# Kernel tuning notes

Measured on AMD Instinct MI355X. Metric: run time of the kernel, lower is better.

The kernel has to match this reference:

```python
import jax, jax.numpy as jnp
import numpy as np

NUM_EXPERTS = 8
HIDDEN = 1024
INTER = 1024
BATCH = 2
SEQ = 1024
TOP_K = 2
SWIGLU_ALPHA = 1.702
LIMIT = 7.0


def setup_inputs() -> dict:
    key = jax.random.key(0)
    ks = jax.random.split(key, 7)
    hidden_states = jax.random.normal(ks[0], (BATCH, SEQ, HIDDEN), jnp.float32)
    router_indices = jax.random.randint(ks[1], (BATCH * SEQ, TOP_K), 0, NUM_EXPERTS)
    routing_weights = jax.nn.softmax(
        jax.random.normal(ks[2], (BATCH * SEQ, NUM_EXPERTS), jnp.float32), axis=-1)
    scale = 0.02
    gate_up_proj = jax.random.normal(ks[3], (NUM_EXPERTS, HIDDEN, 2 * INTER), jnp.float32) * scale
    gate_up_proj_bias = jax.random.normal(ks[4], (NUM_EXPERTS, 2 * INTER), jnp.float32) * scale
    down_proj = jax.random.normal(ks[5], (NUM_EXPERTS, INTER, HIDDEN), jnp.float32) * scale
    down_proj_bias = jax.random.normal(ks[6], (NUM_EXPERTS, HIDDEN), jnp.float32) * scale
    return {
        "hidden_states": hidden_states,
        "router_indices": router_indices,
        "routing_weights": routing_weights,
        "gate_up_proj": gate_up_proj,
        "gate_up_proj_bias": gate_up_proj_bias,
        "down_proj": down_proj,
        "down_proj_bias": down_proj_bias,
    }


def _grouped_mm(x, w, expert_ids):
    """Grouped GEMM: y[t] = x[t] @ w[expert_ids[t]].

    x: [T, K], w: [E, K, N], expert_ids: [T] int.
    Reference form via one-hot masking (exact equivalent of torch._grouped_mm
    on expert-sorted tokens); guaranteed jit- and grad-safe.
    """
    onehot = jax.nn.one_hot(expert_ids, w.shape[0], dtype=x.dtype)  # [T, E]
    y_all = jnp.einsum('tk,ekn->etn', x, w)                         # [E, T, N]
    return jnp.einsum('te,etn->tn', onehot, y_all)                  # [T, N]


def _gpt_oss_swiglu(x):
    gate = jnp.minimum(x[..., ::2], LIMIT)
    up = jnp.clip(x[..., 1::2], -LIMIT, LIMIT)
    glu = gate * jax.nn.sigmoid(gate * SWIGLU_ALPHA)
    return (up + 1.0) * glu


def reference(hidden_states, router_indices, routing_weights,
              gate_up_proj, gate_up_proj_bias, down_proj, down_proj_bias):
    B = hidden_states.shape[0]
    H = hidden_states.shape[-1]
    x = hidden_states.reshape(-1, H)                       # [M, H]
    M = x.shape[0]
    top_k = router_indices.shape[1]
    num_experts = gate_up_proj.shape[0]

    # routing_weights is [M, num_experts] -> gather the top-k weights
    topk_weights = jnp.take_along_axis(routing_weights, router_indices, axis=1)  # [M, K]

    flat_experts = router_indices.reshape(-1)              # [T = M*K]
    sort_idx = jnp.argsort(flat_experts)                   # expert-sorted order
    sorted_pos = sort_idx // top_k                         # token id per slot
    expert_sorted = flat_experts[sort_idx]                 # [T]
    grouped = x[sorted_pos]                                # [T, H]

    gate_up = _grouped_mm(grouped, gate_up_proj, expert_sorted)
    gate_up = gate_up + gate_up_proj_bias[expert_sorted]   # per-expert bias
    inter = _gpt_oss_swiglu(gate_up)                       # [T, I]

    down = _grouped_mm(inter, down_proj, expert_sorted)
    down = down + down_proj_bias[expert_sorted]            # [T, H]
    down = down * topk_weights.reshape(-1)[sort_idx][:, None]

    out = jnp.zeros((M, H), x.dtype).at[sorted_pos].add(down)  # scatter-add combine
    return out.reshape(B, -1, H)
```

## Files before the change

kernel.cpp:

```cpp
#include <hip/hip_runtime.h>

#define NE 8
#define NH 1024
#define NI 1024
#define NGU 2048
#define MTOK 2048
#define TSLOT 4096

#define MAXT64 80
#define MAXT128 40

typedef short s16x8 __attribute__((ext_vector_type(8)));
typedef float f32x4 __attribute__((ext_vector_type(4)));
typedef unsigned short u16;

#define WS_SEG      0
#define WS_DESC64   64
#define WS_DESC128  384
#define WS_SLOT     1024
#define WS_POS      17408
#define WS_INTER    33792
#define WS_AREG     8422400UL
#define WS_WREG     25199616UL
#define WS_DB_OFF   16777216UL
#define WS_NEED_FAST 58754048UL

__device__ inline u16 f2bf(float f) {
    unsigned u = __builtin_bit_cast(unsigned, f);
    u += 0x7fffu + ((u >> 16) & 1u);
    return (u16)(u >> 16);
}

__device__ inline void lds_dma16(const u16* g, u16* l) {
    __builtin_amdgcn_global_load_lds(
        (const __attribute__((address_space(1))) unsigned int*)g,
        (__attribute__((address_space(3))) unsigned int*)l, 16, 0, 0);
}

__device__ inline int lds_off(int row, int blk) {
    return (row << 7) | (((blk ^ (row & 7)) & 7) << 4);
}

__global__ void k_build(const int* __restrict__ ridx, int* __restrict__ seg,
                        int* __restrict__ d64, int* __restrict__ d128,
                        int* __restrict__ slot_of, int* __restrict__ pos_of) {
    __shared__ int cnt[NE];
    __shared__ int cur[NE];
    int tid = threadIdx.x;
    if (tid < NE) cnt[tid] = 0;
    __syncthreads();
    for (int s = tid; s < TSLOT; s += blockDim.x) atomicAdd(&cnt[ridx[s] & 7], 1);
    __syncthreads();
    if (tid == 0) {
        int a = 0;
        for (int e = 0; e < NE; ++e) { seg[e] = a; cur[e] = a; a += cnt[e]; }
        seg[NE] = a;
        int nt = 0;
        for (int e = 0; e < NE; ++e)
            for (int m0 = 0; m0 < cnt[e]; m0 += 64) d64[nt++] = (e << 16) | (m0 / 64);
        for (; nt < MAXT64; ++nt) d64[nt] = -1;
        nt = 0;
        for (int e = 0; e < NE; ++e)
            for (int m0 = 0; m0 < cnt[e]; m0 += 128) d128[nt++] = (e << 16) | (m0 / 128);
        for (; nt < MAXT128; ++nt) d128[nt] = -1;
    }
    __syncthreads();
    for (int s = tid; s < TSLOT; s += blockDim.x) {
        int e = ridx[s] & 7;
        int p = atomicAdd(&cur[e], 1);
        slot_of[p] = s;
        pos_of[s] = p;
    }
}

__global__ __launch_bounds__(256) void k_gather(const float* __restrict__ x,
                                                const int* __restrict__ slot_of,
                                                u16* __restrict__ A) {
    int r = blockIdx.x;
    int token = slot_of[r] >> 1;
    float4 v = ((const float4*)(x + (size_t)token * NH))[threadIdx.x];
    ushort4 o;
    o.x = f2bf(v.x); o.y = f2bf(v.y); o.z = f2bf(v.z); o.w = f2bf(v.w);
    ((ushort4*)(A + (size_t)r * NH))[threadIdx.x] = o;
}

__global__ __launch_bounds__(256) void k_tr(const float* __restrict__ W,
                                            u16* __restrict__ WT, int K, int N) {
    __shared__ u16 T[64][66];
    int tid = threadIdx.x;
    const float* in = W + (size_t)blockIdx.z * K * N;
    u16* out = WT + (size_t)blockIdx.z * N * K;
    int n0 = blockIdx.x * 64, k0 = blockIdx.y * 64;
#pragma unroll
    for (int p = 0; p < 2; ++p) {
        int kr = p * 32 + (tid >> 4) * 2;
        int nc = (tid & 15) * 4;
        const float* r0 = in + (size_t)(k0 + kr) * N + n0 + nc;
        float4 v0 = *(const float4*)r0;
        float4 v1 = *(const float4*)(r0 + N);
#pragma unroll
        for (int i = 0; i < 4; ++i) {
            unsigned lo = f2bf(((const float*)&v0)[i]);
            unsigned hi = f2bf(((const float*)&v1)[i]);
            *(unsigned*)&T[nc + i][kr] = lo | (hi << 16);
        }
    }
    __syncthreads();
#pragma unroll
    for (int p = 0; p < 2; ++p) {
        int idx = p * 256 + tid;
        int nr = idx >> 3, kc = (idx & 7) * 8;
        unsigned q0 = *(const unsigned*)&T[nr][kc + 0];
        unsigned q1 = *(const unsigned*)&T[nr][kc + 2];
        unsigned q2 = *(const unsigned*)&T[nr][kc + 4];
        unsigned q3 = *(const unsigned*)&T[nr][kc + 6];
        uint4 vv = {q0, q1, q2, q3};
        *(uint4*)(out + (size_t)(n0 + nr) * K + k0 + kc) = vv;
    }
}

__global__ __launch_bounds__(256) void k_gateup_f(
        const u16* __restrict__ A,
        const u16* __restrict__ wt,
        const float* __restrict__ bias,
        const int* __restrict__ seg, const int* __restrict__ desc,
        u16* __restrict__ inter) {
    int d = desc[blockIdx.x];
    if (d < 0) return;
    int e = d >> 16, mt = d & 0xffff;
    int seg0 = seg[e], Te = seg[e + 1] - seg0, m0 = mt * 128;

    __shared__ __align__(16) u16 As[128 * 64];
    __shared__ __align__(16) u16 Bs[64 * 64];

    int tid = threadIdx.x;
    int lane = tid & 63, w = tid >> 6;
    int ml = lane & 15, kq = lane >> 4;
    int wm = w >> 1, wn = w & 1;
    int n0 = blockIdx.y * 64;
    const u16* wte = wt + (size_t)e * NGU * NH;
    int dr = lane >> 3, db = (lane & 7) ^ dr;

    f32x4 zero = {0.f, 0.f, 0.f, 0.f};
    f32x4 acc[4][2];
#pragma unroll
    for (int i = 0; i < 4; ++i) { acc[i][0] = zero; acc[i][1] = zero; }

    for (int kb = 0; kb < NH; kb += 64) {
        __syncthreads();
#pragma unroll
        for (int c = 0; c < 4; ++c) {
            int gr = seg0 + m0 + c * 32 + w * 8 + dr;
            if (gr > TSLOT - 1) gr = TSLOT - 1;
            lds_dma16(A + (size_t)gr * NH + kb + db * 8, As + c * 2048 + w * 512);
        }
#pragma unroll
        for (int c = 0; c < 2; ++c) {
            int row = c * 32 + w * 8 + dr;
            lds_dma16(wte + (size_t)(n0 + row) * NH + kb + db * 8, Bs + c * 2048 + w * 512);
        }
        __syncthreads();

#pragma unroll
        for (int kk = 0; kk < 64; kk += 32) {
            s16x8 af[4], bf[2];
#pragma unroll
            for (int i = 0; i < 4; ++i)
                af[i] = *(const s16x8*)((char*)As + lds_off(wm * 64 + i * 16 + ml, (kk >> 3) + kq));
#pragma unroll
            for (int i = 0; i < 2; ++i)
                bf[i] = *(const s16x8*)((char*)Bs + lds_off(wn * 32 + i * 16 + ml, (kk >> 3) + kq));
#pragma unroll
            for (int mi = 0; mi < 4; ++mi)
#pragma unroll
                for (int ni = 0; ni < 2; ++ni)
                    acc[mi][ni] = __builtin_amdgcn_mfma_f32_16x16x32_bf16(
                        af[mi], bf[ni], acc[mi][ni], 0, 0, 0);
        }
    }

#pragma unroll
    for (int ni = 0; ni < 2; ++ni) {
        int n = n0 + wn * 32 + ni * 16 + ml;
        float bv = bias[e * NGU + n];
#pragma unroll
        for (int mi = 0; mi < 4; ++mi) {
#pragma unroll
            for (int r = 0; r < 4; ++r) {
                float v = acc[mi][ni][r] + bv;
                float pr = __shfl_xor(v, 1, 64);
                float g = (lane & 1) ? pr : v;
                float u = (lane & 1) ? v : pr;
                g = fminf(g, 7.0f);
                u = fminf(fmaxf(u, -7.0f), 7.0f);
                float glu = g / (1.0f + __expf(-1.702f * g));
                float y = (u + 1.0f) * glu;
                int mloc = wm * 64 + mi * 16 + kq * 4 + r;
                if (!(lane & 1) && (m0 + mloc) < Te)
                    inter[(size_t)(seg0 + m0 + mloc) * NI + (n >> 1)] = f2bf(y);
            }
        }
    }
}

__global__ __launch_bounds__(256) void k_down_f(
        const u16* __restrict__ inter,
        const u16* __restrict__ wt,
        const float* __restrict__ bias,
        const int* __restrict__ seg, const int* __restrict__ desc,
        float* __restrict__ dA,
        float* __restrict__ dB) {
    int d = desc[blockIdx.x];
    if (d < 0) return;
    int e = d >> 16, mt = d & 0xffff;
    int seg0 = seg[e], Te = seg[e + 1] - seg0, m0 = mt * 128;
    int kz = blockIdx.z;

    __shared__ __align__(16) u16 As[128 * 64];
    __shared__ __align__(16) u16 Bs[64 * 64];

    int tid = threadIdx.x;
    int lane = tid & 63, w = tid >> 6;
    int ml = lane & 15, kq = lane >> 4;
    int wm = w >> 1, wn = w & 1;
    int n0 = blockIdx.y * 64;
    const u16* wte = wt + (size_t)e * NH * NI;
    int dr = lane >> 3, db = (lane & 7) ^ dr;

    f32x4 zero = {0.f, 0.f, 0.f, 0.f};
    f32x4 acc[4][2];
#pragma unroll
    for (int i = 0; i < 4; ++i) { acc[i][0] = zero; acc[i][1] = zero; }

    int kbeg = kz * (NI / 2);
    for (int kb = kbeg; kb < kbeg + NI / 2; kb += 64) {
        __syncthreads();
#pragma unroll
        for (int c = 0; c < 4; ++c) {
            int gr = seg0 + m0 + c * 32 + w * 8 + dr;
            if (gr > TSLOT - 1) gr = TSLOT - 1;
            lds_dma16(inter + (size_t)gr * NI + kb + db * 8, As + c * 2048 + w * 512);
        }
#pragma unroll
        for (int c = 0; c < 2; ++c) {
            int row = c * 32 + w * 8 + dr;
            lds_dma16(wte + (size_t)(n0 + row) * NI + kb + db * 8, Bs + c * 2048 + w * 512);
        }
        __syncthreads();

#pragma unroll
        for (int kk = 0; kk < 64; kk += 32) {
            s16x8 af[4], bf[2];
#pragma unroll
            for (int i = 0; i < 4; ++i)
                af[i] = *(const s16x8*)((char*)As + lds_off(wm * 64 + i * 16 + ml, (kk >> 3) + kq));
#pragma unroll
            for (int i = 0; i < 2; ++i)
                bf[i] = *(const s16x8*)((char*)Bs + lds_off(wn * 32 + i * 16 + ml, (kk >> 3) + kq));
#pragma unroll
            for (int mi = 0; mi < 4; ++mi)
#pragma unroll
                for (int ni = 0; ni < 2; ++ni)
                    acc[mi][ni] = __builtin_amdgcn_mfma_f32_16x16x32_bf16(
                        af[mi], bf[ni], acc[mi][ni], 0, 0, 0);
        }
    }

    float* dst = kz ? dB : dA;
    float bv[2];
#pragma unroll
    for (int ni = 0; ni < 2; ++ni)
        bv[ni] = (kz == 0) ? bias[e * NH + n0 + wn * 32 + ni * 16 + ml] : 0.0f;

#pragma unroll
    for (int mi = 0; mi < 4; ++mi) {
#pragma unroll
        for (int r = 0; r < 4; ++r) {
            int mloc = wm * 64 + mi * 16 + kq * 4 + r;
            if ((m0 + mloc) < Te) {
                size_t row = (size_t)(seg0 + m0 + mloc);
#pragma unroll
                for (int ni = 0; ni < 2; ++ni) {
                    int n = n0 + wn * 32 + ni * 16 + ml;
                    dst[row * NH + n] = acc[mi][ni][r] + bv[ni];
                }
            }
        }
    }
}

__global__ __launch_bounds__(256) void k_comb(
        const float* __restrict__ dA, const float* __restrict__ dB,
        const float* __restrict__ rw, const int* __restrict__ ridx,
        const int* __restrict__ pos_of, float* __restrict__ out) {
    int t = blockIdx.x;
    int h = threadIdx.x * 4;
    float4 s = {0.f, 0.f, 0.f, 0.f};
#pragma unroll
    for (int k = 0; k < 2; ++k) {
        int slot = t * 2 + k;
        int e = ridx[slot] & 7;
        float wgt = rw[t * NE + e];
        size_t r = (size_t)pos_of[slot];
        float4 a = *(const float4*)(dA + r * NH + h);
        float4 b = *(const float4*)(dB + r * NH + h);
        s.x += wgt * (a.x + b.x);
        s.y += wgt * (a.y + b.y);
        s.z += wgt * (a.z + b.z);
        s.w += wgt * (a.w + b.w);
    }
    *(float4*)(out + (size_t)t * NH + h) = s;
}

__global__ __launch_bounds__(256) void k_gateup_s(
        const float* __restrict__ x, const float* __restrict__ w,
        const float* __restrict__ bias,
        const int* __restrict__ seg, const int* __restrict__ desc,
        const int* __restrict__ slot_of, u16* __restrict__ inter) {
    int d = desc[blockIdx.x];
    if (d < 0) return;
    int e = d >> 16, mt = d & 0xffff;
    int seg0 = seg[e], Te = seg[e + 1] - seg0, m0 = mt * 64;
    __shared__ u16 As[64 * 40];
    __shared__ int tok[64];
    int tid = threadIdx.x;
    if (tid < 64) {
        int m = m0 + tid;
        tok[tid] = (m < Te) ? (slot_of[seg0 + m] >> 1) : -1;
    }
    __syncthreads();
    int lane = tid & 63, wave = tid >> 6;
    int arow = tid >> 2, acol = (tid & 3) * 8;
    int ta = tok[arow];
    int kq = lane >> 4, ml = lane & 15;
    int nb = blockIdx.y * 128 + wave * 32;
    const float* wp = w + (size_t)e * NH * NGU;
    f32x4 zero = {0.f, 0.f, 0.f, 0.f};
    f32x4 acc[4][2];
#pragma unroll
    for (int i = 0; i < 4; ++i) { acc[i][0] = zero; acc[i][1] = zero; }
    for (int kb = 0; kb < NH; kb += 32) {
        float4 a0 = {0, 0, 0, 0}, a1 = {0, 0, 0, 0};
        if (ta >= 0) {
            const float* xp = x + (size_t)ta * NH + kb + acol;
            a0 = *(const float4*)xp; a1 = *(const float4*)(xp + 4);
        }
        s16x8 av;
        av[0] = (short)f2bf(a0.x); av[1] = (short)f2bf(a0.y);
        av[2] = (short)f2bf(a0.z); av[3] = (short)f2bf(a0.w);
        av[4] = (short)f2bf(a1.x); av[5] = (short)f2bf(a1.y);
        av[6] = (short)f2bf(a1.z); av[7] = (short)f2bf(a1.w);
        __syncthreads();
        *(s16x8*)&As[arow * 40 + acol] = av;
        __syncthreads();
        s16x8 afr[4];
#pragma unroll
        for (int msi = 0; msi < 4; ++msi)
            afr[msi] = *(const s16x8*)&As[(msi * 16 + ml) * 40 + kq * 8];
        s16x8 bfr[2];
#pragma unroll
        for (int s = 0; s < 2; ++s) {
            const float* bp = wp + (size_t)(kb + kq * 8) * NGU + nb + s * 16 + ml;
#pragma unroll
            for (int j = 0; j < 8; ++j) bfr[s][j] = (short)f2bf(bp[(size_t)j * NGU]);
        }
#pragma unroll
        for (int msi = 0; msi < 4; ++msi)
#pragma unroll
            for (int s = 0; s < 2; ++s)
                acc[msi][s] = __builtin_amdgcn_mfma_f32_16x16x32_bf16(
                    afr[msi], bfr[s], acc[msi][s], 0, 0, 0);
    }
#pragma unroll
    for (int s = 0; s < 2; ++s) {
        int n = nb + s * 16 + ml;
        float bv = bias[e * NGU + n];
#pragma unroll
        for (int msi = 0; msi < 4; ++msi) {
#pragma unroll
            for (int r = 0; r < 4; ++r) {
                float v = acc[msi][s][r] + bv;
                float pr = __shfl_xor(v, 1, 64);
                float g = (lane & 1) ? pr : v;
                float u = (lane & 1) ? v : pr;
                g = fminf(g, 7.0f);
                u = fminf(fmaxf(u, -7.0f), 7.0f);
                float glu = g / (1.0f + __expf(-1.702f * g));
                float y = (u + 1.0f) * glu;
                int mrow = m0 + msi * 16 + kq * 4 + r;
                if (!(lane & 1) && mrow < Te)
                    inter[(size_t)(seg0 + mrow) * NI + (n >> 1)] = f2bf(y);
            }
        }
    }
}

__global__ __launch_bounds__(256) void k_down_s(
        const u16* __restrict__ inter, const float* __restrict__ w,
        const float* __restrict__ bias, const float* __restrict__ rw,
        const int* __restrict__ seg, const int* __restrict__ desc,
        const int* __restrict__ slot_of, float* __restrict__ out) {
    int d = desc[blockIdx.x];
    if (d < 0) return;
    int e = d >> 16, mt = d & 0xffff;
    int seg0 = seg[e], Te = seg[e + 1] - seg0, m0 = mt * 64;
    __shared__ u16 As[64 * 40];
    int tid = threadIdx.x;
    int lane = tid & 63, wave = tid >> 6;
    int arow = tid >> 2, acol = (tid & 3) * 8;
    bool avalid = (m0 + arow) < Te;
    int kq = lane >> 4, ml = lane & 15;
    int nb = blockIdx.y * 128 + wave * 32;
    const float* wp = w + (size_t)e * NI * NH;
    f32x4 zero = {0.f, 0.f, 0.f, 0.f};
    f32x4 acc[4][2];
#pragma unroll
    for (int i = 0; i < 4; ++i) { acc[i][0] = zero; acc[i][1] = zero; }
    for (int kb = 0; kb < NI; kb += 32) {
        s16x8 av = {0, 0, 0, 0, 0, 0, 0, 0};
        if (avalid) av = *(const s16x8*)(inter + (size_t)(seg0 + m0 + arow) * NI + kb + acol);
        __syncthreads();
        *(s16x8*)&As[arow * 40 + acol] = av;
        __syncthreads();
        s16x8 afr[4];
#pragma unroll
        for (int msi = 0; msi < 4; ++msi)
            afr[msi] = *(const s16x8*)&As[(msi * 16 + ml) * 40 + kq * 8];
        s16x8 bfr[2];
#pragma unroll
        for (int s = 0; s < 2; ++s) {
            const float* bp = wp + (size_t)(kb + kq * 8) * NH + nb + s * 16 + ml;
#pragma unroll
            for (int j = 0; j < 8; ++j) bfr[s][j] = (short)f2bf(bp[(size_t)j * NH]);
        }
#pragma unroll
        for (int msi = 0; msi < 4; ++msi)
#pragma unroll
            for (int s = 0; s < 2; ++s)
                acc[msi][s] = __builtin_amdgcn_mfma_f32_16x16x32_bf16(
                    afr[msi], bfr[s], acc[msi][s], 0, 0, 0);
    }
    float bv[2];
    bv[0] = bias[e * NH + nb + ml];
    bv[1] = bias[e * NH + nb + 16 + ml];
#pragma unroll
    for (int msi = 0; msi < 4; ++msi) {
#pragma unroll
        for (int r = 0; r < 4; ++r) {
            int mrow = m0 + msi * 16 + kq * 4 + r;
            if (mrow < Te) {
                int slot = slot_of[seg0 + mrow];
                int token = slot >> 1;
                float wgt = rw[token * NE + e];
#pragma unroll
                for (int s = 0; s < 2; ++s) {
                    int n = nb + s * 16 + ml;
                    atomicAdd(&out[(size_t)token * NH + n], (acc[msi][s][r] + bv[s]) * wgt);
                }
            }
        }
    }
}

extern "C" void kernel_launch(void* const* d_in, const int* in_sizes, int n_in,
                              void* d_out, int out_size, void* d_ws, size_t ws_size,
                              hipStream_t stream) {
    const float* x   = (const float*)d_in[0];
    const int*   ri  = (const int*)d_in[1];
    const float* rw  = (const float*)d_in[2];
    const float* wgu = (const float*)d_in[3];
    const float* bgu = (const float*)d_in[4];
    const float* wd  = (const float*)d_in[5];
    const float* bd  = (const float*)d_in[6];
    float* out = (float*)d_out;

    char* ws = (char*)d_ws;
    int* seg     = (int*)(ws + WS_SEG);
    int* d64     = (int*)(ws + WS_DESC64);
    int* d128    = (int*)(ws + WS_DESC128);
    int* slot_of = (int*)(ws + WS_SLOT);
    int* pos_of  = (int*)(ws + WS_POS);
    u16* inter   = (u16*)(ws + WS_INTER);

    hipLaunchKernelGGL(k_build, dim3(1), dim3(256), 0, stream, ri, seg, d64, d128,
                       slot_of, pos_of);

    if (ws_size >= WS_NEED_FAST) {
        u16*   aReg = (u16*)(ws + WS_AREG);
        float* dA   = (float*)(ws + WS_AREG);
        u16*   wReg = (u16*)(ws + WS_WREG);
        float* dB   = (float*)(ws + WS_WREG + WS_DB_OFF);

        hipLaunchKernelGGL(k_tr, dim3(NGU / 64, NH / 64, NE), dim3(256), 0, stream,
                           wgu, wReg, NH, NGU);
        hipLaunchKernelGGL(k_gather, dim3(TSLOT), dim3(256), 0, stream, x, slot_of, aReg);
        hipLaunchKernelGGL(k_gateup_f, dim3(MAXT128, NGU / 64), dim3(256), 0, stream,
                           aReg, wReg, bgu, seg, d128, inter);
        hipLaunchKernelGGL(k_tr, dim3(NH / 64, NI / 64, NE), dim3(256), 0, stream,
                           wd, wReg, NI, NH);
        hipLaunchKernelGGL(k_down_f, dim3(MAXT128, NH / 64, 2), dim3(256), 0, stream,
                           inter, wReg, bd, seg, d128, dA, dB);
        hipLaunchKernelGGL(k_comb, dim3(MTOK), dim3(256), 0, stream,
                           dA, dB, rw, ri, pos_of, out);
    } else {
        hipMemsetAsync(out, 0, (size_t)MTOK * NH * sizeof(float), stream);
        hipLaunchKernelGGL(k_gateup_s, dim3(MAXT64, NGU / 128), dim3(256), 0, stream,
                           x, wgu, bgu, seg, d64, slot_of, inter);
        hipLaunchKernelGGL(k_down_s, dim3(MAXT64, NH / 128), dim3(256), 0, stream,
                           inter, wd, bd, rw, seg, d64, slot_of, out);
    }
}
```

Measured before the change: 229.4 us.

## Fuse weight bf16 conversion into GEMM staging and combine via atomic scatter

Removes the separate weight transpose/convert kernels; each GEMM block now loads fp32 weights directly and packs them to bf16 into swizzled shared memory. The down projection drops its K-split and the separate combine kernel, instead applying routing weights and atomically adding into a zeroed output. This eliminates a large intermediate write/read of converted weights and two launches, at the cost of reading fp32 weights (twice the bytes) repeatedly per M-tile, less down-GEMM parallelism, and atomic contention.

```diff
diff --git a/kernel.cpp b/kernel.cpp
--- a/kernel.cpp
+++ b/kernel.cpp
@@ -21,9 +21,7 @@
 #define WS_POS      17408
 #define WS_INTER    33792
 #define WS_AREG     8422400UL
-#define WS_WREG     25199616UL
-#define WS_DB_OFF   16777216UL
-#define WS_NEED_FAST 58754048UL
+#define WS_NEED_FAST 16811008UL
 
 __device__ inline u16 f2bf(float f) {
     unsigned u = __builtin_bit_cast(unsigned, f);
@@ -31,6 +29,12 @@
     return (u16)(u >> 16);
 }
 
+__device__ inline unsigned cvt_pk_bf16(float lo, float hi) {
+    unsigned r;
+    asm("v_cvt_pk_bf16_f32 %0, %1, %2" : "=v"(r) : "v"(lo), "v"(hi));
+    return r;
+}
+
 __device__ inline void lds_dma16(const u16* g, u16* l) {
     __builtin_amdgcn_global_load_lds(
         (const __attribute__((address_space(1))) unsigned int*)g,
@@ -39,6 +43,28 @@
 
 __device__ inline int lds_off(int row, int blk) {
     return (row << 7) | (((blk ^ (row & 7)) & 7) << 4);
+}
+
+template<int N>
+__device__ inline void stageB(const float* __restrict__ wt, u16* __restrict__ Bs, int tid) {
+    int lane = tid & 63, w = tid >> 6;
+    int kr = 2 * (lane & 3) + 8 * ((lane >> 2) & 3);
+    int nc = ((lane >> 4) << 2) + (w << 4);
+    const float* r0 = wt + (size_t)kr * N + nc;
+    float4 v0 = *(const float4*)r0;
+    float4 v1 = *(const float4*)(r0 + N);
+    const float* r1 = r0 + (size_t)32 * N;
+    float4 v2 = *(const float4*)r1;
+    float4 v3 = *(const float4*)(r1 + N);
+    int c0 = kr >> 3, kb2 = (kr & 7) << 1;
+#pragma unroll
+    for (int i = 0; i < 4; ++i) {
+        int n = nc + i;
+        unsigned pk0 = cvt_pk_bf16(((const float*)&v0)[i], ((const float*)&v1)[i]);
+        *(unsigned*)((char*)Bs + (n << 7) + (((c0 ^ (n & 7)) & 7) << 4) + kb2) = pk0;
+        unsigned pk1 = cvt_pk_bf16(((const float*)&v2)[i], ((const float*)&v3)[i]);
+        *(unsigned*)((char*)Bs + (n << 7) + ((((c0 + 4) ^ (n & 7)) & 7) << 4) + kb2) = pk1;
+    }
 }
 
 __global__ void k_build(const int* __restrict__ ridx, int* __restrict__ seg,
@@ -84,44 +110,9 @@
     ((ushort4*)(A + (size_t)r * NH))[threadIdx.x] = o;
 }
 
-__global__ __launch_bounds__(256) void k_tr(const float* __restrict__ W,
-                                            u16* __restrict__ WT, int K, int N) {
-    __shared__ u16 T[64][66];
-    int tid = threadIdx.x;
-    const float* in = W + (size_t)blockIdx.z * K * N;
-    u16* out = WT + (size_t)blockIdx.z * N * K;
-    int n0 = blockIdx.x * 64, k0 = blockIdx.y * 64;
-#pragma unroll
-    for (int p = 0; p < 2; ++p) {
-        int kr = p * 32 + (tid >> 4) * 2;
-        int nc = (tid & 15) * 4;
-        const float* r0 = in + (size_t)(k0 + kr) * N + n0 + nc;
-        float4 v0 = *(const float4*)r0;
-        float4 v1 = *(const float4*)(r0 + N);
-#pragma unroll
-        for (int i = 0; i < 4; ++i) {
-            unsigned lo = f2bf(((const float*)&v0)[i]);
-            unsigned hi = f2bf(((const float*)&v1)[i]);
-            *(unsigned*)&T[nc + i][kr] = lo | (hi << 16);
-        }
-    }
-    __syncthreads();
-#pragma unroll
-    for (int p = 0; p < 2; ++p) {
-        int idx = p * 256 + tid;
-        int nr = idx >> 3, kc = (idx & 7) * 8;
-        unsigned q0 = *(const unsigned*)&T[nr][kc + 0];
-        unsigned q1 = *(const unsigned*)&T[nr][kc + 2];
-        unsigned q2 = *(const unsigned*)&T[nr][kc + 4];
-        unsigned q3 = *(const unsigned*)&T[nr][kc + 6];
-        uint4 vv = {q0, q1, q2, q3};
-        *(uint4*)(out + (size_t)(n0 + nr) * K + k0 + kc) = vv;
-    }
-}
-
 __global__ __launch_bounds__(256) void k_gateup_f(
         const u16* __restrict__ A,
-        const u16* __restrict__ wt,
+        const float* __restrict__ W,
         const float* __restrict__ bias,
         const int* __restrict__ seg, const int* __restrict__ desc,
         u16* __restrict__ inter) {
@@ -138,7 +129,7 @@
     int ml = lane & 15, kq = lane >> 4;
     int wm = w >> 1, wn = w & 1;
     int n0 = blockIdx.y * 64;
-    const u16* wte = wt + (size_t)e * NGU * NH;
+    const float* we = W + (size_t)e * NH * NGU;
     int dr = lane >> 3, db = (lane & 7) ^ dr;
 
     f32x4 zero = {0.f, 0.f, 0.f, 0.f};
@@ -154,11 +145,7 @@
             if (gr > TSLOT - 1) gr = TSLOT - 1;
             lds_dma16(A + (size_t)gr * NH + kb + db * 8, As + c * 2048 + w * 512);
         }
-#pragma unroll
-        for (int c = 0; c < 2; ++c) {
-            int row = c * 32 + w * 8 + dr;
-            lds_dma16(wte + (size_t)(n0 + row) * NH + kb + db * 8, Bs + c * 2048 + w * 512);
-        }
+        stageB<NGU>(we + (size_t)kb * NGU + n0, Bs, tid);
         __syncthreads();
 
 #pragma unroll
@@ -205,26 +192,40 @@
 
 __global__ __launch_bounds__(256) void k_down_f(
         const u16* __restrict__ inter,
-        const u16* __restrict__ wt,
+        const float* __restrict__ W,
         const float* __restrict__ bias,
+        const float* __restrict__ rw,
         const int* __restrict__ seg, const int* __restrict__ desc,
-        float* __restrict__ dA,
-        float* __restrict__ dB) {
+        const int* __restrict__ slot_of,
+        float* __restrict__ out) {
     int d = desc[blockIdx.x];
     if (d < 0) return;
     int e = d >> 16, mt = d & 0xffff;
     int seg0 = seg[e], Te = seg[e + 1] - seg0, m0 = mt * 128;
-    int kz = blockIdx.z;
 
     __shared__ __align__(16) u16 As[128 * 64];
     __shared__ __align__(16) u16 Bs[64 * 64];
+    __shared__ int tokS[128];
+    __shared__ float wgtS[128];
 
     int tid = threadIdx.x;
+    if (tid < 128) {
+        int m = m0 + tid;
+        if (m < Te) {
+            int token = slot_of[seg0 + m] >> 1;
+            tokS[tid] = token;
+            wgtS[tid] = rw[token * NE + e];
+        } else {
+            tokS[tid] = 0;
+            wgtS[tid] = 0.0f;
+        }
+    }
+
     int lane = tid & 63, w = tid >> 6;
     int ml = lane & 15, kq = lane >> 4;
     int wm = w >> 1, wn = w & 1;
     int n0 = blockIdx.y * 64;
-    const u16* wte = wt + (size_t)e * NH * NI;
+    const float* we = W + (size_t)e * NI * NH;
     int dr = lane >> 3, db = (lane & 7) ^ dr;
 
     f32x4 zero = {0.f, 0.f, 0.f, 0.f};
@@ -232,8 +233,7 @@
 #pragma unroll
     for (int i = 0; i < 4; ++i) { acc[i][0] = zero; acc[i][1] = zero; }
 
-    int kbeg = kz * (NI / 2);
-    for (int kb = kbeg; kb < kbeg + NI / 2; kb += 64) {
+    for (int kb = 0; kb < NI; kb += 64) {
         __syncthreads();
 #pragma unroll
         for (int c = 0; c < 4; ++c) {
@@ -241,11 +241,7 @@
             if (gr > TSLOT - 1) gr = TSLOT - 1;
             lds_dma16(inter + (size_t)gr * NI + kb + db * 8, As + c * 2048 + w * 512);
         }
-#pragma unroll
-        for (int c = 0; c < 2; ++c) {
-            int row = c * 32 + w * 8 + dr;
-            lds_dma16(wte + (size_t)(n0 + row) * NI + kb + db * 8, Bs + c * 2048 + w * 512);
-        }
+        stageB<NH>(we + (size_t)kb * NH + n0, Bs, tid);
         __syncthreads();
 
 #pragma unroll
@@ -266,11 +262,10 @@
         }
     }
 
-    float* dst = kz ? dB : dA;
     float bv[2];
 #pragma unroll
     for (int ni = 0; ni < 2; ++ni)
-        bv[ni] = (kz == 0) ? bias[e * NH + n0 + wn * 32 + ni * 16 + ml] : 0.0f;
+        bv[ni] = bias[e * NH + n0 + wn * 32 + ni * 16 + ml];
 
 #pragma unroll
     for (int mi = 0; mi < 4; ++mi) {
@@ -278,38 +273,16 @@
         for (int r = 0; r < 4; ++r) {
             int mloc = wm * 64 + mi * 16 + kq * 4 + r;
             if ((m0 + mloc) < Te) {
-                size_t row = (size_t)(seg0 + m0 + mloc);
+                int token = tokS[mloc];
+                float wgt = wgtS[mloc];
 #pragma unroll
                 for (int ni = 0; ni < 2; ++ni) {
                     int n = n0 + wn * 32 + ni * 16 + ml;
-                    dst[row * NH + n] = acc[mi][ni][r] + bv[ni];
+                    atomicAdd(&out[(size_t)token * NH + n], (acc[mi][ni][r] + bv[ni]) * wgt);
                 }
             }
         }
     }
-}
-
-__global__ __launch_bounds__(256) void k_comb(
-        const float* __restrict__ dA, const float* __restrict__ dB,
-        const float* __restrict__ rw, const int* __restrict__ ridx,
-        const int* __restrict__ pos_of, float* __restrict__ out) {
-    int t = blockIdx.x;
-    int h = threadIdx.x * 4;
-    float4 s = {0.f, 0.f, 0.f, 0.f};
-#pragma unroll
-    for (int k = 0; k < 2; ++k) {
-        int slot = t * 2 + k;
-        int e = ridx[slot] & 7;
-        float wgt = rw[t * NE + e];
-        size_t r = (size_t)pos_of[slot];
-        float4 a = *(const float4*)(dA + r * NH + h);
-        float4 b = *(const float4*)(dB + r * NH + h);
-        s.x += wgt * (a.x + b.x);
-        s.y += wgt * (a.y + b.y);
-        s.z += wgt * (a.z + b.z);
-        s.w += wgt * (a.w + b.w);
-    }
-    *(float4*)(out + (size_t)t * NH + h) = s;
 }
 
 __global__ __launch_bounds__(256) void k_gateup_s(
@@ -484,26 +457,16 @@
 
     hipLaunchKernelGGL(k_build, dim3(1), dim3(256), 0, stream, ri, seg, d64, d128,
                        slot_of, pos_of);
+    hipMemsetAsync(out, 0, (size_t)MTOK * NH * sizeof(float), stream);
 
     if (ws_size >= WS_NEED_FAST) {
-        u16*   aReg = (u16*)(ws + WS_AREG);
-        float* dA   = (float*)(ws + WS_AREG);
-        u16*   wReg = (u16*)(ws + WS_WREG);
-        float* dB   = (float*)(ws + WS_WREG + WS_DB_OFF);
-
-        hipLaunchKernelGGL(k_tr, dim3(NGU / 64, NH / 64, NE), dim3(256), 0, stream,
-                           wgu, wReg, NH, NGU);
+        u16* aReg = (u16*)(ws + WS_AREG);
         hipLaunchKernelGGL(k_gather, dim3(TSLOT), dim3(256), 0, stream, x, slot_of, aReg);
         hipLaunchKernelGGL(k_gateup_f, dim3(MAXT128, NGU / 64), dim3(256), 0, stream,
-                           aReg, wReg, bgu, seg, d128, inter);
-        hipLaunchKernelGGL(k_tr, dim3(NH / 64, NI / 64, NE), dim3(256), 0, stream,
-                           wd, wReg, NI, NH);
-        hipLaunchKernelGGL(k_down_f, dim3(MAXT128, NH / 64, 2), dim3(256), 0, stream,
-                           inter, wReg, bd, seg, d128, dA, dB);
-        hipLaunchKernelGGL(k_comb, dim3(MTOK), dim3(256), 0, stream,
-                           dA, dB, rw, ri, pos_of, out);
+                           aReg, wgu, bgu, seg, d128, inter);
+        hipLaunchKernelGGL(k_down_f, dim3(MAXT128, NH / 64), dim3(256), 0, stream,
+                           inter, wd, bd, rw, seg, d128, slot_of, out);
     } else {
-        hipMemsetAsync(out, 0, (size_t)MTOK * NH * sizeof(float), stream);
         hipLaunchKernelGGL(k_gateup_s, dim3(MAXT64, NGU / 128), dim3(256), 0, stream,
                            x, wgu, bgu, seg, d64, slot_of, inter);
         hipLaunchKernelGGL(k_down_s, dim3(MAXT64, NH / 128), dim3(256), 0, stream,
```

After: 269.7 us. +17.6%, slower.

## Widen GEMM N-tile to 128 and fuse weighted combine into down kernel via atomics

Applied to the files above, without the earlier changes.

Both bf16 grouped GEMMs move from 128x64 to 128x128 output tiles, so each wave now holds a 4x4 MFMA accumulator grid and each loaded A tile is reused across twice as many columns. The down projection drops its split-K over two halves and the separate fp32 partial buffers. It now applies the routing weight and scatter-adds straight into the output with atomicAdd, which removes the k_comb kernel and its round trip through global memory. In exchange the output needs a memset, there are fewer blocks for parallelism, register pressure is higher, and the fp32 atomics make the summation order nondeterministic.

```diff
diff --git a/kernel.cpp b/kernel.cpp
--- a/kernel.cpp
+++ b/kernel.cpp
@@ -22,7 +22,6 @@
 #define WS_INTER    33792
 #define WS_AREG     8422400UL
 #define WS_WREG     25199616UL
-#define WS_DB_OFF   16777216UL
 #define WS_NEED_FAST 58754048UL
 
 __device__ inline u16 f2bf(float f) {
@@ -131,20 +130,22 @@
     int seg0 = seg[e], Te = seg[e + 1] - seg0, m0 = mt * 128;
 
     __shared__ __align__(16) u16 As[128 * 64];
-    __shared__ __align__(16) u16 Bs[64 * 64];
+    __shared__ __align__(16) u16 Bs[128 * 64];
 
     int tid = threadIdx.x;
     int lane = tid & 63, w = tid >> 6;
     int ml = lane & 15, kq = lane >> 4;
     int wm = w >> 1, wn = w & 1;
-    int n0 = blockIdx.y * 64;
+    int n0 = blockIdx.y * 128;
     const u16* wte = wt + (size_t)e * NGU * NH;
     int dr = lane >> 3, db = (lane & 7) ^ dr;
 
     f32x4 zero = {0.f, 0.f, 0.f, 0.f};
-    f32x4 acc[4][2];
-#pragma unroll
-    for (int i = 0; i < 4; ++i) { acc[i][0] = zero; acc[i][1] = zero; }
+    f32x4 acc[4][4];
+#pragma unroll
+    for (int i = 0; i < 4; ++i)
+#pragma unroll
+        for (int j = 0; j < 4; ++j) acc[i][j] = zero;
 
     for (int kb = 0; kb < NH; kb += 64) {
         __syncthreads();
@@ -155,7 +156,7 @@
             lds_dma16(A + (size_t)gr * NH + kb + db * 8, As + c * 2048 + w * 512);
         }
 #pragma unroll
-        for (int c = 0; c < 2; ++c) {
+        for (int c = 0; c < 4; ++c) {
             int row = c * 32 + w * 8 + dr;
             lds_dma16(wte + (size_t)(n0 + row) * NH + kb + db * 8, Bs + c * 2048 + w * 512);
         }
@@ -163,25 +164,25 @@
 
 #pragma unroll
         for (int kk = 0; kk < 64; kk += 32) {
-            s16x8 af[4], bf[2];
+            s16x8 af[4], bf[4];
 #pragma unroll
             for (int i = 0; i < 4; ++i)
                 af[i] = *(const s16x8*)((char*)As + lds_off(wm * 64 + i * 16 + ml, (kk >> 3) + kq));
 #pragma unroll
-            for (int i = 0; i < 2; ++i)
-                bf[i] = *(const s16x8*)((char*)Bs + lds_off(wn * 32 + i * 16 + ml, (kk >> 3) + kq));
+            for (int i = 0; i < 4; ++i)
+                bf[i] = *(const s16x8*)((char*)Bs + lds_off(wn * 64 + i * 16 + ml, (kk >> 3) + kq));
 #pragma unroll
             for (int mi = 0; mi < 4; ++mi)
 #pragma unroll
-                for (int ni = 0; ni < 2; ++ni)
+                for (int ni = 0; ni < 4; ++ni)
                     acc[mi][ni] = __builtin_amdgcn_mfma_f32_16x16x32_bf16(
                         af[mi], bf[ni], acc[mi][ni], 0, 0, 0);
         }
     }
 
 #pragma unroll
-    for (int ni = 0; ni < 2; ++ni) {
-        int n = n0 + wn * 32 + ni * 16 + ml;
+    for (int ni = 0; ni < 4; ++ni) {
+        int n = n0 + wn * 64 + ni * 16 + ml;
         float bv = bias[e * NGU + n];
 #pragma unroll
         for (int mi = 0; mi < 4; ++mi) {
@@ -207,33 +208,48 @@
         const u16* __restrict__ inter,
         const u16* __restrict__ wt,
         const float* __restrict__ bias,
+        const float* __restrict__ rw,
         const int* __restrict__ seg, const int* __restrict__ desc,
-        float* __restrict__ dA,
-        float* __restrict__ dB) {
+        const int* __restrict__ slot_of,
+        float* __restrict__ out) {
     int d = desc[blockIdx.x];
     if (d < 0) return;
     int e = d >> 16, mt = d & 0xffff;
     int seg0 = seg[e], Te = seg[e + 1] - seg0, m0 = mt * 128;
-    int kz = blockIdx.z;
 
     __shared__ __align__(16) u16 As[128 * 64];
-    __shared__ __align__(16) u16 Bs[64 * 64];
+    __shared__ __align__(16) u16 Bs[128 * 64];
+    __shared__ int tokS[128];
+    __shared__ float wgtS[128];
 
     int tid = threadIdx.x;
+    if (tid < 128) {
+        int m = m0 + tid;
+        if (m < Te) {
+            int token = slot_of[seg0 + m] >> 1;
+            tokS[tid] = token;
+            wgtS[tid] = rw[token * NE + e];
+        } else {
+            tokS[tid] = 0;
+            wgtS[tid] = 0.0f;
+        }
+    }
+
     int lane = tid & 63, w = tid >> 6;
     int ml = lane & 15, kq = lane >> 4;
     int wm = w >> 1, wn = w & 1;
-    int n0 = blockIdx.y * 64;
+    int n0 = blockIdx.y * 128;
     const u16* wte = wt + (size_t)e * NH * NI;
     int dr = lane >> 3, db = (lane & 7) ^ dr;
 
     f32x4 zero = {0.f, 0.f, 0.f, 0.f};
-    f32x4 acc[4][2];
-#pragma unroll
-    for (int i = 0; i < 4; ++i) { acc[i][0] = zero; acc[i][1] = zero; }
-
-    int kbeg = kz * (NI / 2);
-    for (int kb = kbeg; kb < kbeg + NI / 2; kb += 64) {
+    f32x4 acc[4][4];
+#pragma unroll
+    for (int i = 0; i < 4; ++i)
+#pragma unroll
+        for (int j = 0; j < 4; ++j) acc[i][j] = zero;
+
+    for (int kb = 0; kb < NI; kb += 64) {
         __syncthreads();
 #pragma unroll
         for (int c = 0; c < 4; ++c) {
@@ -242,7 +258,7 @@
             lds_dma16(inter + (size_t)gr * NI + kb + db * 8, As + c * 2048 + w * 512);
         }
 #pragma unroll
-        for (int c = 0; c < 2; ++c) {
+        for (int c = 0; c < 4; ++c) {
             int row = c * 32 + w * 8 + dr;
             lds_dma16(wte + (size_t)(n0 + row) * NI + kb + db * 8, Bs + c * 2048 + w * 512);
         }
@@ -250,27 +266,26 @@
 
 #pragma unroll
         for (int kk = 0; kk < 64; kk += 32) {
-            s16x8 af[4], bf[2];
+            s16x8 af[4], bf[4];
 #pragma unroll
             for (int i = 0; i < 4; ++i)
                 af[i] = *(const s16x8*)((char*)As + lds_off(wm * 64 + i * 16 + ml, (kk >> 3) + kq));
 #pragma unroll
-            for (int i = 0; i < 2; ++i)
-                bf[i] = *(const s16x8*)((char*)Bs + lds_off(wn * 32 + i * 16 + ml, (kk >> 3) + kq));
+            for (int i = 0; i < 4; ++i)
+                bf[i] = *(const s16x8*)((char*)Bs + lds_off(wn * 64 + i * 16 + ml, (kk >> 3) + kq));
 #pragma unroll
             for (int mi = 0; mi < 4; ++mi)
 #pragma unroll
-                for (int ni = 0; ni < 2; ++ni)
+                for (int ni = 0; ni < 4; ++ni)
                     acc[mi][ni] = __builtin_amdgcn_mfma_f32_16x16x32_bf16(
                         af[mi], bf[ni], acc[mi][ni], 0, 0, 0);
         }
     }
 
-    float* dst = kz ? dB : dA;
-    float bv[2];
-#pragma unroll
-    for (int ni = 0; ni < 2; ++ni)
-        bv[ni] = (kz == 0) ? bias[e * NH + n0 + wn * 32 + ni * 16 + ml] : 0.0f;
+    float bv[4];
+#pragma unroll
+    for (int ni = 0; ni < 4; ++ni)
+        bv[ni] = bias[e * NH + n0 + wn * 64 + ni * 16 + ml];
 
 #pragma unroll
     for (int mi = 0; mi < 4; ++mi) {
@@ -278,38 +293,16 @@
         for (int r = 0; r < 4; ++r) {
             int mloc = wm * 64 + mi * 16 + kq * 4 + r;
             if ((m0 + mloc) < Te) {
-                size_t row = (size_t)(seg0 + m0 + mloc);
-#pragma unroll
-                for (int ni = 0; ni < 2; ++ni) {
-                    int n = n0 + wn * 32 + ni * 16 + ml;
-                    dst[row * NH + n] = acc[mi][ni][r] + bv[ni];
+                int token = tokS[mloc];
+                float wgt = wgtS[mloc];
+#pragma unroll
+                for (int ni = 0; ni < 4; ++ni) {
+                    int n = n0 + wn * 64 + ni * 16 + ml;
+                    atomicAdd(&out[(size_t)token * NH + n], (acc[mi][ni][r] + bv[ni]) * wgt);
                 }
             }
         }
     }
-}
-
-__global__ __launch_bounds__(256) void k_comb(
-        const float* __restrict__ dA, const float* __restrict__ dB,
-        const float* __restrict__ rw, const int* __restrict__ ridx,
-        const int* __restrict__ pos_of, float* __restrict__ out) {
-    int t = blockIdx.x;
-    int h = threadIdx.x * 4;
-    float4 s = {0.f, 0.f, 0.f, 0.f};
-#pragma unroll
-    for (int k = 0; k < 2; ++k) {
-        int slot = t * 2 + k;
-        int e = ridx[slot] & 7;
-        float wgt = rw[t * NE + e];
-        size_t r = (size_t)pos_of[slot];
-        float4 a = *(const float4*)(dA + r * NH + h);
-        float4 b = *(const float4*)(dB + r * NH + h);
-        s.x += wgt * (a.x + b.x);
-        s.y += wgt * (a.y + b.y);
-        s.z += wgt * (a.z + b.z);
-        s.w += wgt * (a.w + b.w);
-    }
-    *(float4*)(out + (size_t)t * NH + h) = s;
 }
 
 __global__ __launch_bounds__(256) void k_gateup_s(
@@ -484,26 +477,21 @@
 
     hipLaunchKernelGGL(k_build, dim3(1), dim3(256), 0, stream, ri, seg, d64, d128,
                        slot_of, pos_of);
+    hipMemsetAsync(out, 0, (size_t)MTOK * NH * sizeof(float), stream);
 
     if (ws_size >= WS_NEED_FAST) {
-        u16*   aReg = (u16*)(ws + WS_AREG);
-        float* dA   = (float*)(ws + WS_AREG);
-        u16*   wReg = (u16*)(ws + WS_WREG);
-        float* dB   = (float*)(ws + WS_WREG + WS_DB_OFF);
-
+        u16* aReg = (u16*)(ws + WS_AREG);
+        u16* wReg = (u16*)(ws + WS_WREG);
         hipLaunchKernelGGL(k_tr, dim3(NGU / 64, NH / 64, NE), dim3(256), 0, stream,
                            wgu, wReg, NH, NGU);
         hipLaunchKernelGGL(k_gather, dim3(TSLOT), dim3(256), 0, stream, x, slot_of, aReg);
-        hipLaunchKernelGGL(k_gateup_f, dim3(MAXT128, NGU / 64), dim3(256), 0, stream,
+        hipLaunchKernelGGL(k_gateup_f, dim3(MAXT128, NGU / 128), dim3(256), 0, stream,
                            aReg, wReg, bgu, seg, d128, inter);
         hipLaunchKernelGGL(k_tr, dim3(NH / 64, NI / 64, NE), dim3(256), 0, stream,
                            wd, wReg, NI, NH);
-        hipLaunchKernelGGL(k_down_f, dim3(MAXT128, NH / 64, 2), dim3(256), 0, stream,
-                           inter, wReg, bd, seg, d128, dA, dB);
-        hipLaunchKernelGGL(k_comb, dim3(MTOK), dim3(256), 0, stream,
-                           dA, dB, rw, ri, pos_of, out);
+        hipLaunchKernelGGL(k_down_f, dim3(MAXT128, NH / 128), dim3(256), 0, stream,
+                           inter, wReg, bd, rw, seg, d128, slot_of, out);
     } else {
-        hipMemsetAsync(out, 0, (size_t)MTOK * NH * sizeof(float), stream);
         hipLaunchKernelGGL(k_gateup_s, dim3(MAXT64, NGU / 128), dim3(256), 0, stream,
                            x, wgu, bgu, seg, d64, slot_of, inter);
         hipLaunchKernelGGL(k_down_s, dim3(MAXT64, NH / 128), dim3(256), 0, stream,
```

Result: slower. 251.8 us (+9.8%).
